# Kernel tuning notes

Measured on AMD Instinct MI355X. Metric: run time of the kernel, lower is better.

Reference implementation:

```python
import jax, jax.numpy as jnp
import numpy as np
from jax import lax

# (name, low, high) in the j-order used to index feature_correction[:, j]
LIMITS = [("f_start", 0.5, 5.0), ("f_inf", 0.01, 0.5), ("f_decay", 0.0, 2.0),
          ("f_T", 0.0, 2.0), ("w_offset", 0.0, 1.0), ("w_T", 0.01, 0.5)]
BN_EPS = 1e-5


def _batchnorm(x, g, b):
    # training-mode BatchNorm1d: biased batch stats over the batch dim
    m = jnp.mean(x, axis=0)
    v = jnp.var(x, axis=0)
    return (x - m) * jax.lax.rsqrt(v + BN_EPS) * g + b


def setup_inputs() -> dict:
    key = jax.random.key(0)
    ks = jax.random.split(key, 16)
    B, T, NF, NH, NP = 2048, 4096, 32, 8, 6
    X = jax.random.normal(ks[0], (B, T), dtype=jnp.float32)
    features = jax.random.normal(ks[1], (B, NF), dtype=jnp.float32)
    F = jnp.float32(1.0)

    def lin(k, fin, fout):
        kw, kb = jax.random.split(k)
        s = 1.0 / np.sqrt(fin)
        W = jax.random.uniform(kw, (fout, fin), minval=-s, maxval=s, dtype=jnp.float32)
        b = jax.random.uniform(kb, (fout,), minval=-s, maxval=s, dtype=jnp.float32)
        return W, b

    W1, b1 = lin(ks[2], NF, NH)
    W2, b2 = lin(ks[3], NH, NH)
    W3, b3 = lin(ks[4], NH, NP)
    bn0_g = 1.0 + 0.1 * jax.random.normal(ks[5], (NF,), dtype=jnp.float32)
    bn0_b = 0.1 * jax.random.normal(ks[6], (NF,), dtype=jnp.float32)
    bn1_g = 1.0 + 0.1 * jax.random.normal(ks[7], (NH,), dtype=jnp.float32)
    bn1_b = 0.1 * jax.random.normal(ks[8], (NH,), dtype=jnp.float32)
    bn2_g = 1.0 + 0.1 * jax.random.normal(ks[9], (NH,), dtype=jnp.float32)
    bn2_b = 0.1 * jax.random.normal(ks[10], (NH,), dtype=jnp.float32)
    param_normals = 0.5 * jax.random.normal(ks[11], (NP,), dtype=jnp.float32)
    return {"X": X, "features": features, "F": F,
            "bn0_g": bn0_g, "bn0_b": bn0_b, "W1": W1, "b1": b1,
            "bn1_g": bn1_g, "bn1_b": bn1_b, "W2": W2, "b2": b2,
            "bn2_g": bn2_g, "bn2_b": bn2_b, "W3": W3, "b3": b3,
            "param_normals": param_normals}


def reference(X, features, F, bn0_g, bn0_b, W1, b1, bn1_g, bn1_b,
              W2, b2, bn2_g, bn2_b, W3, b3, param_normals):
    B, T = X.shape
    # MLP: BN -> Linear -> BN -> ReLU -> Linear -> BN -> ReLU -> Linear
    h = _batchnorm(features, bn0_g, bn0_b)
    h = h @ W1.T + b1
    h = jax.nn.relu(_batchnorm(h, bn1_g, bn1_b))
    h = h @ W2.T + b2
    h = jax.nn.relu(_batchnorm(h, bn2_g, bn2_b))
    corr = h @ W3.T + b3  # [B, 6]

    p = {}
    for j, (name, lo, hi) in enumerate(LIMITS):
        p[name] = lo + (hi - lo) * jax.nn.sigmoid(corr[:, j] + param_normals[j])
        p[name] = p[name][:, None]  # [B, 1]

    t = (jnp.arange(T, dtype=jnp.float32) / T)[None, :]  # [1, T]
    f = p["f_inf"] + (p["f_start"] - p["f_inf"]) * \
        (0.7 * 0.1 ** p["f_decay"]) ** (t / (10.0 * 0.1 ** p["f_T"]))  # [B, T]
    w = jax.nn.sigmoid((t - p["w_offset"]) / p["w_T"])  # [B, T]
    c = np.sqrt(2.0 ** (1.0 / 3.0) - 1.0) * F / np.pi
    a = (f - c) / (f + c)
    b = (a + 1.0) * 0.5

    # original detaches X at every step -> recurrence sees stop_gradient(X)
    X0 = lax.stop_gradient(X)
    y0 = X0[:, 0]  # y1[0] = y2[0] = X[:, 0]

    def step(carry, inp):
        y1p, y2p, xp = carry
        x_t, a_t, b_t = inp
        y1 = b_t * (x_t + xp) - a_t * y1p
        y2 = b_t * (y1 + y1p) - a_t * y2p
        return (y1, y2, x_t), y2

    xs = (X0[:, 1:].T, a[:, 1:].T, b[:, 1:].T)  # each [T-1, B]
    _, ys = lax.scan(step, (y0, y0, y0), xs)
    y2_all = jnp.concatenate([y0[None, :], ys], axis=0)  # [T, B]

    averaged_summed = jnp.sum(w.T * y2_all, axis=0)  # [B]
    normalization = jnp.sum(w, axis=1)  # [B]
    prediction = averaged_summed / normalization
    return prediction
```

## Files before the change

### kernel.cpp

```cpp
#include <hip/hip_runtime.h>
#include <hip/hip_bf16.h>
#include <math.h>

#define NF 32
#define NH 8
#define NP 6

__global__ __launch_bounds__(256) void moments_kernel(
    const float* __restrict__ feat,
    float* __restrict__ mu,
    float* __restrict__ S,
    int B)
{
    const int i = blockIdx.x;
    const int tid = threadIdx.x;
    float s = 0.f;
    float sj[NF];
#pragma unroll
    for (int j = 0; j < NF; j++) sj[j] = 0.f;

    for (int r = tid; r < B; r += 256) {
        const float* row = feat + (size_t)r * NF;
        const float4* row4 = (const float4*)row;
        float fi = row[i];
        s += fi;
#pragma unroll
        for (int jq = 0; jq < NF / 4; jq++) {
            float4 q = row4[jq];
            sj[4*jq+0] = fmaf(fi, q.x, sj[4*jq+0]);
            sj[4*jq+1] = fmaf(fi, q.y, sj[4*jq+1]);
            sj[4*jq+2] = fmaf(fi, q.z, sj[4*jq+2]);
            sj[4*jq+3] = fmaf(fi, q.w, sj[4*jq+3]);
        }
    }
#pragma unroll
    for (int d = 1; d < 64; d <<= 1) {
        s += __shfl_xor(s, d);
#pragma unroll
        for (int j = 0; j < NF; j++) sj[j] += __shfl_xor(sj[j], d);
    }
    __shared__ float red[4][NF + 1];
    const int wv = tid >> 6, lane = tid & 63;
    if (lane == 0) {
#pragma unroll
        for (int j = 0; j < NF; j++) red[wv][j] = sj[j];
        red[wv][NF] = s;
    }
    __syncthreads();
    if (tid < NF + 1) {
        float tot = red[0][tid] + red[1][tid] + red[2][tid] + red[3][tid];
        tot *= (1.0f / (float)B);
        if (tid < NF) S[(size_t)i * NF + tid] = tot;
        else mu[i] = tot;
    }
}

__global__ __launch_bounds__(256) void mlp_kernel(
    const float* __restrict__ feat,
    const float* __restrict__ mu,
    const float* __restrict__ S,
    const float* __restrict__ bn0_g, const float* __restrict__ bn0_b,
    const float* __restrict__ W1, const float* __restrict__ b1,
    const float* __restrict__ bn1_g, const float* __restrict__ bn1_b,
    const float* __restrict__ W2, const float* __restrict__ b2,
    float* __restrict__ h2buf,
    float* __restrict__ part,
    int B)
{
    __shared__ float ssc0[NF], ssh0[NF], smu[NF];
    __shared__ float w1p[NH][NF];
    __shared__ float Wf[NH][NF];
    __shared__ float bfold[NH];
    __shared__ float sW2[NH * NH], sb2[NH];
    __shared__ float vgrp[8];
    __shared__ float ssc1[NH];

    const int tid = threadIdx.x;
    if (tid < NF) {
        float m = mu[tid];
        smu[tid] = m;
        float var = S[(size_t)tid * NF + tid] - m * m;
        float sc = bn0_g[tid] * rsqrtf(var + 1e-5f);
        ssc0[tid] = sc;
        ssh0[tid] = bn0_b[tid] - m * sc;
    }
    if (tid >= 64 && tid < 64 + NH * NH) sW2[tid - 64] = W2[tid - 64];
    if (tid >= 128 && tid < 128 + NH) sb2[tid - 128] = b2[tid - 128];
    __syncthreads();
    {
        const int o = tid >> 5, i = tid & 31;
        w1p[o][i] = W1[o * NF + i] * ssc0[i];
    }
    __syncthreads();
    float vacc;
    {
        const int o = tid >> 5, i = tid & 31;
        float mi = smu[i];
        float acc = 0.f;
#pragma unroll
        for (int j = 0; j < NF; j++)
            acc = fmaf(S[(size_t)i * NF + j] - mi * smu[j], w1p[o][j], acc);
        vacc = acc * w1p[o][i];
    }
#pragma unroll
    for (int d = 1; d < 32; d <<= 1) vacc += __shfl_xor(vacc, d, 32);
    if ((tid & 31) == 0) vgrp[tid >> 5] = vacc;
    __syncthreads();
    if (tid < NH) {
        const int o = tid;
        float c1 = b1[o];
#pragma unroll
        for (int i = 0; i < NF; i++) c1 = fmaf(W1[o * NF + i], ssh0[i], c1);
        float m1 = c1;
#pragma unroll
        for (int i = 0; i < NF; i++) m1 = fmaf(w1p[o][i], smu[i], m1);
        float var1 = vgrp[o];
        float sc1 = bn1_g[o] * rsqrtf(var1 + 1e-5f);
        float sh1 = bn1_b[o] - m1 * sc1;
        ssc1[o] = sc1;
        bfold[o] = fmaf(sc1, c1, sh1);
    }
    __syncthreads();
    {
        const int o = tid >> 5, i = tid & 31;
        Wf[o][i] = ssc1[o] * w1p[o][i];
    }
    __syncthreads();

    const int r = blockIdx.x * 256 + tid;
    float h[NH];
    if (r < B) {
        float x[NF];
        const float4* row4 = (const float4*)(feat + (size_t)r * NF);
#pragma unroll
        for (int jq = 0; jq < NF / 4; jq++) {
            float4 q = row4[jq];
            x[4*jq+0] = q.x; x[4*jq+1] = q.y; x[4*jq+2] = q.z; x[4*jq+3] = q.w;
        }
        float x2[NH];
#pragma unroll
        for (int o = 0; o < NH; o++) {
            float z = bfold[o];
#pragma unroll
            for (int i = 0; i < NF; i++) z = fmaf(Wf[o][i], x[i], z);
            x2[o] = fmaxf(z, 0.f);
        }
#pragma unroll
        for (int o = 0; o < NH; o++) {
            float acc = sb2[o];
#pragma unroll
            for (int i = 0; i < NH; i++) acc = fmaf(sW2[o * NH + i], x2[i], acc);
            h[o] = acc;
            h2buf[(size_t)r * NH + o] = acc;
        }
    } else {
#pragma unroll
        for (int o = 0; o < NH; o++) h[o] = 0.f;
    }

    __shared__ float ls[NH][256];
    __shared__ float lq[NH][256];
#pragma unroll
    for (int o = 0; o < NH; o++) { ls[o][tid] = h[o]; lq[o][tid] = h[o] * h[o]; }
    __syncthreads();
    for (int st = 128; st > 0; st >>= 1) {
        if (tid < st) {
#pragma unroll
            for (int o = 0; o < NH; o++) {
                ls[o][tid] += ls[o][tid + st];
                lq[o][tid] += lq[o][tid + st];
            }
        }
        __syncthreads();
    }
    if (tid < NH) {
        part[(size_t)blockIdx.x * 2 * NH + tid] = ls[tid][0];
        part[(size_t)blockIdx.x * 2 * NH + NH + tid] = lq[tid][0];
    }
}

__global__ __launch_bounds__(256) void scan_kernel(
    const float* __restrict__ X,
    const float* __restrict__ h2buf,
    const float* __restrict__ part,
    const float* __restrict__ bn2_g, const float* __restrict__ bn2_b,
    const float* __restrict__ W3, const float* __restrict__ b3,
    const float* __restrict__ pn,
    const float* __restrict__ Fp,
    float* __restrict__ out, int B, int T, int nb)
{
    __shared__ float ssc2[NH], ssh2[NH];
    __shared__ float sW3[NP * NH], sb3[NP], spn[NP];
    __shared__ float sF;
    const int tid = threadIdx.x;
    if (tid < NH) {
        float s = 0.f, q = 0.f;
        for (int c = 0; c < nb; c++) {
            s += part[(size_t)c * 2 * NH + tid];
            q += part[(size_t)c * 2 * NH + NH + tid];
        }
        float inv_n = 1.0f / (float)B;
        float m = s * inv_n;
        float var = q * inv_n - m * m;
        float sc = bn2_g[tid] * rsqrtf(var + 1e-5f);
        ssc2[tid] = sc;
        ssh2[tid] = bn2_b[tid] - m * sc;
    }
    if (tid >= 64 && tid < 64 + NP * NH) sW3[tid - 64] = W3[tid - 64];
    if (tid >= 128 && tid < 128 + NP) sb3[tid - 128] = b3[tid - 128];
    if (tid >= 160 && tid < 160 + NP) spn[tid - 160] = pn[tid - 160];
    if (tid == 192) sF = Fp[0];
    __syncthreads();

    const int lane = tid & 63;
    const int r = blockIdx.x * 4 + (tid >> 6);
    if (r >= B) return;

    float x3[NH];
#pragma unroll
    for (int i = 0; i < NH; i++) {
        float v = h2buf[(size_t)r * NH + i] * ssc2[i] + ssh2[i];
        x3[i] = fmaxf(v, 0.0f);
    }
    const float lo[NP] = {0.5f, 0.01f, 0.0f, 0.0f, 0.0f, 0.01f};
    const float hi[NP] = {5.0f, 0.5f, 2.0f, 2.0f, 1.0f, 0.5f};
    float p[NP];
#pragma unroll
    for (int j = 0; j < NP; j++) {
        float cr = sb3[j] + spn[j];
#pragma unroll
        for (int i = 0; i < NH; i++) cr = fmaf(sW3[j * NH + i], x3[i], cr);
        float sg = 1.0f / (1.0f + expf(-cr));
        p[j] = lo[j] + (hi[j] - lo[j]) * sg;
    }
    const float f_inf = p[1], df = p[0] - p[1];
    const float LOG2_0p7 = -0.5145731728297583f;
    const float LOG2_0p1 = -3.3219280948873623f;
    const float LOG2_10 = 3.3219280948873623f;
    float log2base = LOG2_0p7 + p[2] * LOG2_0p1;
    float invden = 0.1f * exp2f(LOG2_10 * p[3]);
    const float k = log2base * invden / (float)T;
    const float wsc = 1.0f / ((float)T * p[5]);
    const float wb = -p[4] / p[5];
    const float c = sqrtf(exp2f(1.0f / 3.0f) - 1.0f) * sF * (1.0f / 3.14159265358979323846f);
    const float c2 = 2.0f * c;

    const int C = T >> 6;
    const int t0 = lane * C;
    const float* Xr = X + (size_t)r * T;
    const float4* Xr4 = (const float4*)(Xr + t0);
    const float ek = exp2f(k);
    const float er = expf(-wsc);

    float e = exp2f(k * (float)t0);
    float E = expf(-(wsc * (float)t0 + wb));
    float xp = (lane == 0) ? 0.f : Xr[t0 - 1];

    float P = 1.f, Q = 0.f, V1 = 0.f, V2 = 0.f;
    float A1 = 0.f, A2 = 0.f, A0 = 0.f, wsum = 0.f;

    for (int j = 0; j < C / 4; j++) {
        float4 xq = Xr4[j];
        float xs[4] = {xq.x, xq.y, xq.z, xq.w};
#pragma unroll
        for (int m = 0; m < 4; m++) {
            const int t = t0 + j * 4 + m;
            const float x = xs[m];
            if (t == 0) {
                P = 0.f; Q = 0.f; V1 = x; V2 = x;
            } else {
                float ft = fmaf(df, e, f_inf);
                float inv = __builtin_amdgcn_rcpf(ft + c);
                float a = fmaf(-c2, inv, 1.0f);
                float b = fmaf(-c, inv, 1.0f);
                float u = b * (x + xp);
                float g = b * c2 * inv;
                float Pn = -a * P;
                float Qn = fmaf(g, P, -a * Q);
                float V1n = fmaf(-a, V1, u);
                float V2n = fmaf(g, V1, fmaf(-a, V2, b * u));
                P = Pn; Q = Qn; V1 = V1n; V2 = V2n;
            }
            float w = __builtin_amdgcn_rcpf(1.0f + E);
            A1 = fmaf(w, Q, A1);
            A2 = fmaf(w, P, A2);
            A0 = fmaf(w, V2, A0);
            wsum += w;
            e *= ek;
            E *= er;
            xp = x;
        }
    }

#pragma unroll
    for (int d = 1; d < 64; d <<= 1) {
        float Po = __shfl_up(P, d);
        float Qo = __shfl_up(Q, d);
        float V1o = __shfl_up(V1, d);
        float V2o = __shfl_up(V2, d);
        if (lane >= d) {
            float Pn = P * Po;
            float Qn = fmaf(Q, Po, P * Qo);
            float V1n = fmaf(P, V1o, V1);
            float V2n = fmaf(Q, V1o, fmaf(P, V2o, V2));
            P = Pn; Q = Qn; V1 = V1n; V2 = V2n;
        }
    }
    float y1in = __shfl_up(V1, 1);
    float y2in = __shfl_up(V2, 1);
    if (lane == 0) { y1in = 0.f; y2in = 0.f; }

    float contrib = fmaf(A1, y1in, fmaf(A2, y2in, A0));
#pragma unroll
    for (int d = 1; d < 64; d <<= 1) {
        contrib += __shfl_xor(contrib, d);
        wsum += __shfl_xor(wsum, d);
    }
    if (lane == 0) out[r] = contrib / wsum;
}

extern "C" void kernel_launch(void* const* d_in, const int* in_sizes, int n_in,
                              void* d_out, int out_size, void* d_ws, size_t ws_size,
                              hipStream_t stream) {
    const float* X = (const float*)d_in[0];
    const float* features = (const float*)d_in[1];
    const float* Fp = (const float*)d_in[2];
    const float* bn0_g = (const float*)d_in[3];
    const float* bn0_b = (const float*)d_in[4];
    const float* W1 = (const float*)d_in[5];
    const float* b1 = (const float*)d_in[6];
    const float* bn1_g = (const float*)d_in[7];
    const float* bn1_b = (const float*)d_in[8];
    const float* W2 = (const float*)d_in[9];
    const float* b2 = (const float*)d_in[10];
    const float* bn2_g = (const float*)d_in[11];
    const float* bn2_b = (const float*)d_in[12];
    const float* W3 = (const float*)d_in[13];
    const float* b3 = (const float*)d_in[14];
    const float* pn = (const float*)d_in[15];
    float* out = (float*)d_out;

    const int B = in_sizes[1] / NF;
    const int T = in_sizes[0] / B;
    const int nb = (B + 255) / 256;

    float* ws = (float*)d_ws;
    float* mu = ws;
    float* S = ws + NF;
    float* part = S + NF * NF;
    float* h2buf = part + (size_t)nb * 16;

    moments_kernel<<<NF, 256, 0, stream>>>(features, mu, S, B);
    mlp_kernel<<<nb, 256, 0, stream>>>(features, mu, S, bn0_g, bn0_b, W1, b1,
                                       bn1_g, bn1_b, W2, b2, h2buf, part, B);
    scan_kernel<<<(B + 3) / 4, 256, 0, stream>>>(X, h2buf, part, bn2_g, bn2_b,
                                                 W3, b3, pn, Fp, out, B, T, nb);
}
```

Measured before the change: 41.50 us.

## Split each row's scan across a full 256-thread block with cross-wave composition

Each row is now handled by one 256-thread block instead of one 64-lane wavefront. Every thread scans a chunk of T/256 steps, and the per-wave affine scan aggregates are combined through shared memory. The final weighted sum is also reduced across waves through shared memory. This cuts the serial per-thread chain length by four and raises the block count, at the cost of two extra block barriers, a redundant per-row MLP head in every wave, and 2048 blocks instead of 512.

```diff
diff --git a/kernel.cpp b/kernel.cpp
--- a/kernel.cpp
+++ b/kernel.cpp
@@ -192,6 +192,8 @@
     __shared__ float ssc2[NH], ssh2[NH];
     __shared__ float sW3[NP * NH], sb3[NP], spn[NP];
     __shared__ float sF;
+    __shared__ float wcomp[4][4];
+    __shared__ float rsum[4][2];
     const int tid = threadIdx.x;
     if (tid < NH) {
         float s = 0.f, q = 0.f;
@@ -212,9 +214,9 @@
     if (tid == 192) sF = Fp[0];
     __syncthreads();
 
+    const int r = blockIdx.x;
     const int lane = tid & 63;
-    const int r = blockIdx.x * 4 + (tid >> 6);
-    if (r >= B) return;
+    const int wv = tid >> 6;
 
     float x3[NH];
 #pragma unroll
@@ -245,8 +247,8 @@
     const float c = sqrtf(exp2f(1.0f / 3.0f) - 1.0f) * sF * (1.0f / 3.14159265358979323846f);
     const float c2 = 2.0f * c;
 
-    const int C = T >> 6;
-    const int t0 = lane * C;
+    const int C = T >> 8;
+    const int t0 = tid * C;
     const float* Xr = X + (size_t)r * T;
     const float4* Xr4 = (const float4*)(Xr + t0);
     const float ek = exp2f(k);
@@ -254,7 +256,7 @@
 
     float e = exp2f(k * (float)t0);
     float E = expf(-(wsc * (float)t0 + wb));
-    float xp = (lane == 0) ? 0.f : Xr[t0 - 1];
+    float xp = (tid == 0) ? 0.f : Xr[t0 - 1];
 
     float P = 1.f, Q = 0.f, V1 = 0.f, V2 = 0.f;
     float A1 = 0.f, A2 = 0.f, A0 = 0.f, wsum = 0.f;
@@ -306,9 +308,28 @@
             P = Pn; Q = Qn; V1 = V1n; V2 = V2n;
         }
     }
-    float y1in = __shfl_up(V1, 1);
-    float y2in = __shfl_up(V2, 1);
-    if (lane == 0) { y1in = 0.f; y2in = 0.f; }
+
+    if (lane == 63) {
+        wcomp[wv][0] = P; wcomp[wv][1] = Q; wcomp[wv][2] = V1; wcomp[wv][3] = V2;
+    }
+
+    float Pe = __shfl_up(P, 1);
+    float Qe = __shfl_up(Q, 1);
+    float V1e = __shfl_up(V1, 1);
+    float V2e = __shfl_up(V2, 1);
+    if (lane == 0) { Pe = 1.f; Qe = 0.f; V1e = 0.f; V2e = 0.f; }
+    __syncthreads();
+
+    float y1s = 0.f, y2s = 0.f;
+    for (int i = 0; i < wv; i++) {
+        float Pi = wcomp[i][0], Qi = wcomp[i][1], V1i = wcomp[i][2], V2i = wcomp[i][3];
+        float y1n = fmaf(Pi, y1s, V1i);
+        float y2n = fmaf(Qi, y1s, fmaf(Pi, y2s, V2i));
+        y1s = y1n; y2s = y2n;
+    }
+
+    float y1in = fmaf(Pe, y1s, V1e);
+    float y2in = fmaf(Qe, y1s, fmaf(Pe, y2s, V2e));
 
     float contrib = fmaf(A1, y1in, fmaf(A2, y2in, A0));
 #pragma unroll
@@ -316,7 +337,13 @@
         contrib += __shfl_xor(contrib, d);
         wsum += __shfl_xor(wsum, d);
     }
-    if (lane == 0) out[r] = contrib / wsum;
+    if (lane == 0) { rsum[wv][0] = contrib; rsum[wv][1] = wsum; }
+    __syncthreads();
+    if (tid == 0) {
+        float ct = rsum[0][0] + rsum[1][0] + rsum[2][0] + rsum[3][0];
+        float wt = rsum[0][1] + rsum[1][1] + rsum[2][1] + rsum[3][1];
+        out[r] = ct / wt;
+    }
 }
 
 extern "C" void kernel_launch(void* const* d_in, const int* in_sizes, int n_in,
@@ -353,6 +380,6 @@
     moments_kernel<<<NF, 256, 0, stream>>>(features, mu, S, B);
     mlp_kernel<<<nb, 256, 0, stream>>>(features, mu, S, bn0_g, bn0_b, W1, b1,
                                        bn1_g, bn1_b, W2, b2, h2buf, part, B);
-    scan_kernel<<<(B + 3) / 4, 256, 0, stream>>>(X, h2buf, part, bn2_g, bn2_b,
-                                                 W3, b3, pn, Fp, out, B, T, nb);
+    scan_kernel<<<B, 256, 0, stream>>>(X, h2buf, part, bn2_g, bn2_b,
+                                       W3, b3, pn, Fp, out, B, T, nb);
 }
```

After: 43.89 us. +5.8%, slower.
